# Optimization experiments

Hardware: AMD Instinct MI355X
Metric: run time of the kernel (lower is better)

Reference implementation:

```python
import jax, jax.numpy as jnp
import numpy as np

B = 8192
E = 8
H = 128
NUM_CLASSES = 3
SIM_THRESHOLD = 0.8
EFF_THRESHOLD = 0.1
TARGET_TEMP = 1.0
W_LB, W_EFF, W_CONS, W_ENT, W_TEMP = 0.1, 0.05, 0.1, 0.01, 0.01


def setup_inputs() -> dict:
    key = jax.random.key(0)
    k1, k2, k3, k4 = jax.random.split(key, 4)
    logits = jax.random.normal(k1, (B, NUM_CLASSES), dtype=jnp.float32)
    targets = jax.random.randint(k2, (B,), 0, NUM_CLASSES, dtype=jnp.int64)
    raw = jax.random.uniform(k3, (B, E), dtype=jnp.float32)
    routing_probs = raw / raw.sum(axis=-1, keepdims=True)  # rows sum to 1
    input_embeddings = jax.random.uniform(k4, (B, H), dtype=jnp.float32)
    temperature = jnp.ones((1,), dtype=jnp.float32)
    return {
        "logits": logits,
        "targets": targets,
        "routing_probs": routing_probs,
        "input_embeddings": input_embeddings,
        "temperature": temperature,
    }


def _dynamo_loss(logits, routing_probs, input_embeddings, temperature, targets):
    # --- task loss: cross entropy (sentiment) ---
    logp_cls = jax.nn.log_softmax(logits, axis=-1)
    task_loss = -jnp.take_along_axis(logp_cls, targets[:, None], axis=-1).mean()

    # --- load balance: var(mean usage) / (1/E)^2 (torch.var unbiased) ---
    expert_usage = routing_probs.mean(axis=0)  # [E]
    lb_loss = W_LB * jnp.var(expert_usage, ddof=1) * (E ** 2)

    # --- efficiency: sum of probs below threshold, averaged over batch ---
    small = jnp.where(routing_probs < EFF_THRESHOLD, routing_probs, 0.0)
    eff_loss = W_EFF * small.sum(axis=-1).mean()

    # --- consistency: masked pairwise KL over similar samples ---
    nrm = input_embeddings / jnp.linalg.norm(input_embeddings, axis=-1, keepdims=True)
    sim = nrm @ nrm.T  # [B, B]
    mask = (sim > SIM_THRESHOLD) & ~jnp.eye(B, dtype=bool)
    logp = jax.nn.log_softmax(routing_probs, axis=-1)  # [B, E]
    p = jnp.exp(logp)
    a = jnp.sum(p * logp, axis=-1)  # [B], sum_e p_j log p_j
    # KL(i,j) = sum_e p_j (log p_j - log p_i) = a[j] - logp[i] . p[j]
    kl = a[None, :] - logp @ p.T  # [B, B]
    num_pairs = mask.sum()
    kl_sum = jnp.sum(jnp.where(mask, kl, 0.0))
    cons_loss = W_CONS * jnp.where(num_pairs > 0, kl_sum / jnp.maximum(num_pairs, 1), 0.0)

    # --- entropy regularization (maximize entropy of routing_probs-as-probs) ---
    eps = 1e-8
    entropy = -jnp.sum(routing_probs * jnp.log(routing_probs + eps), axis=-1)
    ent_loss = W_ENT * (-entropy.mean())

    # --- temperature regularization ---
    temp_loss = W_TEMP * jnp.mean((temperature - TARGET_TEMP) ** 2)

    return task_loss + lb_loss + eff_loss + cons_loss + ent_loss + temp_loss


def reference(logits, targets, routing_probs, input_embeddings, temperature):
    return _dynamo_loss(logits, routing_probs, input_embeddings, temperature, targets)
```

## Files before the change

### kernel.cpp

```cpp
#include <hip/hip_runtime.h>
#include <stdint.h>

#define B_SZ 8192
#define LOG8 2.0794415416798357f
#define NTILE 2080

typedef __attribute__((ext_vector_type(8))) short short8;
typedef __attribute__((ext_vector_type(4))) float floatx4;

typedef __attribute__((address_space(1))) const uint4 guint4;
typedef __attribute__((address_space(3))) uint4 luint4;

__device__ inline void async_cp16(const uint4* g, uint4* l) {
    __builtin_amdgcn_global_load_lds((guint4*)g, (luint4*)l, 16, 0, 0);
}

__device__ inline unsigned short f2bf(float f) {
    unsigned int u = __float_as_uint(f);
    u = (u + 0x7FFFu + ((u >> 16) & 1u)) >> 16;
    return (unsigned short)u;
}
__device__ inline float bf2f(unsigned short s) {
    return __uint_as_float(((unsigned int)s) << 16);
}
__device__ inline float wredf(float x) {
#pragma unroll
    for (int o = 32; o; o >>= 1) x += __shfl_down(x, o);
    return x;
}
__device__ inline int wredi(int x) {
#pragma unroll
    for (int o = 32; o; o >>= 1) x += __shfl_down(x, o);
    return x;
}


__global__ __launch_bounds__(512) void prep_all(
    const float* __restrict__ logits,
    const int* __restrict__ targets,
    const float* __restrict__ routing,
    const float* __restrict__ emb,
    unsigned short* __restrict__ nrm,
    unsigned short* __restrict__ nlq,
    unsigned short* __restrict__ pb,
    float* __restrict__ aprime,
    float* __restrict__ prepslot) {
    __shared__ float pred[8][11];
    const int bid = blockIdx.x;
    const int lane = threadIdx.x & 63;
    const int wave = threadIdx.x >> 6;

    if (bid < 256) {
#pragma unroll
        for (int iter = 0; iter < 4; ++iter) {
            int row = (((iter << 8) + bid) << 3) + wave;
            const float2* e2 = (const float2*)(emb + (size_t)row * 128);
            float2 v = e2[lane];
            float ss = v.x * v.x + v.y * v.y;
            ss = wredf(ss);
            ss = __shfl(ss, 0);
            float inv = rsqrtf(ss);
            ushort2 o;
            o.x = f2bf(v.x * inv);
            o.y = f2bf(v.y * inv);
            ((ushort2*)(nrm + (size_t)row * 128))[lane] = o;
        }
        return;
    }

    int row = ((bid - 256) << 9) + threadIdx.x;

    const float4* r4 = (const float4*)(routing + (size_t)row * 8);
    float4 va = r4[0], vb = r4[1];
    float v[8] = {va.x, va.y, va.z, va.w, vb.x, vb.y, vb.z, vb.w};

    float mx = v[0];
#pragma unroll
    for (int e = 1; e < 8; ++e) mx = fmaxf(mx, v[e]);
    float ex[8], s = 0.f;
#pragma unroll
    for (int e = 0; e < 8; ++e) { ex[e] = expf(v[e] - mx); s += ex[e]; }
    float ls = logf(s);
    float inv_s = 1.f / s;

    union { unsigned short u[8]; uint4 q; } lu, pu;
    float ap = 0.f;
#pragma unroll
    for (int e = 0; e < 8; ++e) {
        unsigned short pe = f2bf(ex[e] * inv_s);
        unsigned short le = f2bf(v[e] - mx - ls + LOG8);
        pu.u[e] = pe;
        lu.u[e] = le ^ 0x8000;
        ap += bf2f(pe) * bf2f(le);
    }
    ((uint4*)nlq)[row] = lu.q;
    ((uint4*)pb)[row] = pu.q;
    aprime[row] = ap;

    float eff = 0.f, ent = 0.f;
#pragma unroll
    for (int e = 0; e < 8; ++e) {
        if (v[e] < 0.1f) eff += v[e];
        ent += v[e] * logf(v[e] + 1e-8f);
    }

    const float* lg = logits + (size_t)row * 3;
    float a0 = lg[0], a1 = lg[1], a2 = lg[2];
    float mm = fmaxf(a0, fmaxf(a1, a2));
    float lse = mm + logf(expf(a0 - mm) + expf(a1 - mm) + expf(a2 - mm));
    int tg = targets[row];
    float tv = (tg == 0) ? a0 : ((tg == 1) ? a1 : a2);
    float task = lse - tv;

    task = wredf(task);
    eff = wredf(eff);
    ent = wredf(ent);
    float cs[8];
#pragma unroll
    for (int e = 0; e < 8; ++e) cs[e] = wredf(v[e]);

    if (lane == 0) {
        pred[wave][0] = task;
        pred[wave][1] = eff;
        pred[wave][2] = ent;
#pragma unroll
        for (int e = 0; e < 8; ++e) pred[wave][3 + e] = cs[e];
    }
    __syncthreads();
    if (threadIdx.x < 11) {
        float s2 = 0.f;
#pragma unroll
        for (int w = 0; w < 8; ++w) s2 += pred[w][threadIdx.x];
        prepslot[(bid - 256) * 11 + threadIdx.x] = s2;
    }
}

__global__ __launch_bounds__(512, 4) void tile_sym(
    const unsigned short* __restrict__ nrm,
    const unsigned short* __restrict__ nlq,
    const unsigned short* __restrict__ pb,
    const float* __restrict__ aprime,
    float* __restrict__ klslot,
    unsigned int* __restrict__ cntslot) {
    __shared__ uint4 sh[2048];

    const int t = threadIdx.x;
    const int L = blockIdx.x;
    const int wave = t >> 6, lane = t & 63;

    int bi = (int)((129.0f - sqrtf((float)(16641 - 8 * L))) * 0.5f);
    int T = bi * 64 - ((bi * (bi - 1)) >> 1);
    while (L < T) { --bi; T = bi * 64 - ((bi * (bi - 1)) >> 1); }
    while (L >= T + (64 - bi)) { T += 64 - bi; ++bi; }
    const int bj = bi + (L - T);
    const bool diag = (bi == bj);
    const int iBase = bi << 7, jBase = bj << 7;

    const uint4* n4 = (const uint4*)nrm;

#pragma unroll
    for (int it = 0; it < 4; ++it) {
        int idx = t + (it << 9);
        int row = idx >> 4, s = idx & 15;
        int g = s ^ (row & 15);
        async_cp16(&n4[((size_t)(iBase + row) << 4) + g],
                   sh + (it << 9) + (wave << 6));
    }

    const int wr = wave >> 2, wc = wave & 3;
    const int m = lane & 15, q = lane >> 4;

    const int colB0 = jBase + (wc << 5) + m;
    short8 bfr[4][2];
#pragma unroll
    for (int ks = 0; ks < 4; ++ks)
#pragma unroll
        for (int b = 0; b < 2; ++b)
            bfr[ks][b] = *(const short8*)&nrm[(size_t)(colB0 + (b << 4)) * 128 +
                                              (ks << 5) + (q << 3)];

    __syncthreads();

    floatx4 simacc[4][2];
#pragma unroll
    for (int a = 0; a < 4; ++a)
#pragma unroll
        for (int b = 0; b < 2; ++b) simacc[a][b] = (floatx4){0.f, 0.f, 0.f, 0.f};

#pragma unroll
    for (int ks = 0; ks < 4; ++ks) {
        const int gk = (ks << 2) + q;
        short8 af[4];
#pragma unroll
        for (int a = 0; a < 4; ++a) {
            int row = (wr << 6) + (a << 4) + m;
            af[a] = *(const short8*)(sh + (row << 4) + (gk ^ m));
        }
#pragma unroll
        for (int a = 0; a < 4; ++a)
#pragma unroll
            for (int b = 0; b < 2; ++b)
                simacc[a][b] = __builtin_amdgcn_mfma_f32_16x16x32_bf16(
                    af[a], bfr[ks][b], simacc[a][b], 0, 0, 0);
    }

    const short8 zero8 = (short8){0, 0, 0, 0, 0, 0, 0, 0};
    short8 crA[4], crB[2];
#pragma unroll
    for (int a = 0; a < 4; ++a) {
        int ri = iBase + (wr << 6) + (a << 4) + m;
        short8 v = zero8;
        if (q == 0) v = *(const short8*)&nlq[(size_t)ri << 3];
        else if (q == 1) { if (!diag) v = *(const short8*)&pb[(size_t)ri << 3]; }
        else if (q == 2) {
            v[1] = (short)0x3F80;
            if (!diag) v[0] = (short)f2bf(aprime[ri]);
        }
        crA[a] = v;
    }
#pragma unroll
    for (int b = 0; b < 2; ++b) {
        int cj = jBase + (wc << 5) + (b << 4) + m;
        short8 v = zero8;
        if (q == 0) v = *(const short8*)&pb[(size_t)cj << 3];
        else if (q == 1) v = *(const short8*)&nlq[(size_t)cj << 3];
        else if (q == 2) {
            v[0] = (short)0x3F80;
            v[1] = (short)f2bf(aprime[cj]);
        }
        crB[b] = v;
    }

    float klLocal = 0.f;
    int cntLocal = 0;
#pragma unroll
    for (int a = 0; a < 4; ++a) {
        const int gRow0 = iBase + (wr << 6) + (a << 4) + (q << 2);
#pragma unroll
        for (int b = 0; b < 2; ++b) {
            const int gCol = jBase + (wc << 5) + (b << 4) + m;
            floatx4 cr = __builtin_amdgcn_mfma_f32_16x16x32_bf16(
                crA[a], crB[b], (floatx4){0.f, 0.f, 0.f, 0.f}, 0, 0, 0);
            if (diag) {
#pragma unroll
                for (int r = 0; r < 4; ++r) {
                    if ((simacc[a][b][r] > 0.8f) && (gRow0 + r != gCol)) {
                        klLocal += cr[r];
                        cntLocal += 1;
                    }
                }
            } else {
#pragma unroll
                for (int r = 0; r < 4; ++r) {
                    if (simacc[a][b][r] > 0.8f) {
                        klLocal += cr[r];
                        cntLocal += 2;
                    }
                }
            }
        }
    }

    klLocal = wredf(klLocal);
    cntLocal = wredi(cntLocal);

    __syncthreads();
    float* redk = (float*)sh;
    int* redc = (int*)(redk + 8);
    if (lane == 0) { redk[wave] = klLocal; redc[wave] = cntLocal; }
    __syncthreads();

    if (t == 0) {
        float k = 0.f;
        int c = 0;
#pragma unroll
        for (int w = 0; w < 8; ++w) { k += redk[w]; c += redc[w]; }
        klslot[L] = k;
        cntslot[L] = (unsigned int)c;
    }
}

__global__ void finalize_k(const float* __restrict__ klslot,
                           const unsigned int* __restrict__ cntslot,
                           const float* __restrict__ prepslot,
                           const float* __restrict__ temp,
                           float* __restrict__ out) {
    __shared__ float sk[4];
    __shared__ int sc[4];
    __shared__ float sp[11];
    const int t = threadIdx.x, lane = t & 63, wave = t >> 6;

    float k = 0.f;
    int c = 0;
    for (int i = t; i < NTILE; i += 256) { k += klslot[i]; c += (int)cntslot[i]; }
    k = wredf(k);
    c = wredi(c);
    if (lane == 0) { sk[wave] = k; sc[wave] = c; }
    if (t < 11) {
        float s = 0.f;
        for (int r = 0; r < 16; ++r) s += prepslot[r * 11 + t];
        sp[t] = s;
    }
    __syncthreads();
    if (t == 0) {
        float K = sk[0] + sk[1] + sk[2] + sk[3];
        int C = sc[0] + sc[1] + sc[2] + sc[3];
        const float invB = 1.f / (float)B_SZ;
        float task = sp[0] * invB;
        float eff = 0.05f * sp[1] * invB;
        float entl = 0.01f * sp[2] * invB;
        float cons = 0.1f * (C > 0 ? K / (float)C : 0.f);
        float u[8], mean = 0.f;
        for (int e = 0; e < 8; ++e) { u[e] = sp[3 + e] * invB; mean += u[e]; }
        mean *= 0.125f;
        float var = 0.f;
        for (int e = 0; e < 8; ++e) { float d = u[e] - mean; var += d * d; }
        var *= (1.f / 7.f);
        float lb = 0.1f * var * 64.f;
        float tt = temp[0] - 1.f;
        out[0] = task + lb + eff + cons + entl + 0.01f * tt * tt;
    }
}

extern "C" void kernel_launch(void* const* d_in, const int* in_sizes, int n_in,
                              void* d_out, int out_size, void* d_ws, size_t ws_size,
                              hipStream_t stream) {
    const float* logits = (const float*)d_in[0];
    const int* targets = (const int*)d_in[1];
    const float* routing = (const float*)d_in[2];
    const float* emb = (const float*)d_in[3];
    const float* temp = (const float*)d_in[4];

    char* ws = (char*)d_ws;
    unsigned short* nrm = (unsigned short*)ws;
    unsigned short* nlq = (unsigned short*)(ws + 2097152);
    unsigned short* pb = (unsigned short*)(ws + 2228224);
    float* aprime = (float*)(ws + 2359296);
    float* klslot = (float*)(ws + 2392064);
    unsigned int* cntslot = (unsigned int*)(ws + 2400384);
    float* prepslot = (float*)(ws + 2408704);

    prep_all<<<272, 512, 0, stream>>>(logits, targets, routing, emb,
                                      nrm, nlq, pb, aprime, prepslot);
    tile_sym<<<NTILE, 512, 0, stream>>>(nrm, nlq, pb, aprime, klslot, cntslot);
    finalize_k<<<1, 256, 0, stream>>>(klslot, cntslot, prepslot, temp,
                                      (float*)d_out);
}
```

Measured before the change: 107.2 us.

## Halve column tile width and stage B operand in shared memory

The symmetric tile grid changes from 128x128 tiles to 128x64 tiles, which doubles the block count. The column rows of the normalized embeddings are now loaded into LDS with async copies instead of directly into registers from global memory. Tile index decoding is rewritten for the new triangular-strip layout, with a 'strip' flag replacing the diagonal flag, and the slot offsets in the workspace are shifted to fit the larger block count. The aim is more parallelism and less register pressure, at the cost of more blocks, redundant A-tile loads, and more partial-sum slots to reduce.

```diff
diff --git a/kernel.cpp b/kernel.cpp
--- a/kernel.cpp
+++ b/kernel.cpp
@@ -3,7 +3,7 @@
 
 #define B_SZ 8192
 #define LOG8 2.0794415416798357f
-#define NTILE 2080
+#define NTILE 4160
 
 typedef __attribute__((ext_vector_type(8))) short short8;
 typedef __attribute__((ext_vector_type(4))) float floatx4;
@@ -142,19 +142,19 @@
     const float* __restrict__ aprime,
     float* __restrict__ klslot,
     unsigned int* __restrict__ cntslot) {
-    __shared__ uint4 sh[2048];
+    __shared__ uint4 sh[3072];
 
     const int t = threadIdx.x;
     const int L = blockIdx.x;
     const int wave = t >> 6, lane = t & 63;
 
-    int bi = (int)((129.0f - sqrtf((float)(16641 - 8 * L))) * 0.5f);
-    int T = bi * 64 - ((bi * (bi - 1)) >> 1);
-    while (L < T) { --bi; T = bi * 64 - ((bi * (bi - 1)) >> 1); }
-    while (L >= T + (64 - bi)) { T += 64 - bi; ++bi; }
-    const int bj = bi + (L - T);
-    const bool diag = (bi == bj);
-    const int iBase = bi << 7, jBase = bj << 7;
+    int bi = (int)((129.0f - sqrtf((float)(16641 - 4 * L))) * 0.5f);
+    int T = bi * (129 - bi);
+    while (L < T) { --bi; T = bi * (129 - bi); }
+    while (L >= T + (128 - 2 * bi)) { T += 128 - 2 * bi; ++bi; }
+    const int bj = 2 * bi + (L - T);
+    const bool strip = ((bj >> 1) == bi);
+    const int iBase = bi << 7, jBase = bj << 6;
 
     const uint4* n4 = (const uint4*)nrm;
 
@@ -166,61 +166,34 @@
         async_cp16(&n4[((size_t)(iBase + row) << 4) + g],
                    sh + (it << 9) + (wave << 6));
     }
+#pragma unroll
+    for (int it = 0; it < 2; ++it) {
+        int idx = t + (it << 9);
+        int row = idx >> 4, s = idx & 15;
+        int g = s ^ (row & 15);
+        async_cp16(&n4[((size_t)(jBase + row) << 4) + g],
+                   sh + 2048 + (it << 9) + (wave << 6));
+    }
 
     const int wr = wave >> 2, wc = wave & 3;
     const int m = lane & 15, q = lane >> 4;
-
-    const int colB0 = jBase + (wc << 5) + m;
-    short8 bfr[4][2];
-#pragma unroll
-    for (int ks = 0; ks < 4; ++ks)
-#pragma unroll
-        for (int b = 0; b < 2; ++b)
-            bfr[ks][b] = *(const short8*)&nrm[(size_t)(colB0 + (b << 4)) * 128 +
-                                              (ks << 5) + (q << 3)];
-
-    __syncthreads();
-
-    floatx4 simacc[4][2];
-#pragma unroll
-    for (int a = 0; a < 4; ++a)
-#pragma unroll
-        for (int b = 0; b < 2; ++b) simacc[a][b] = (floatx4){0.f, 0.f, 0.f, 0.f};
-
-#pragma unroll
-    for (int ks = 0; ks < 4; ++ks) {
-        const int gk = (ks << 2) + q;
-        short8 af[4];
-#pragma unroll
-        for (int a = 0; a < 4; ++a) {
-            int row = (wr << 6) + (a << 4) + m;
-            af[a] = *(const short8*)(sh + (row << 4) + (gk ^ m));
-        }
-#pragma unroll
-        for (int a = 0; a < 4; ++a)
-#pragma unroll
-            for (int b = 0; b < 2; ++b)
-                simacc[a][b] = __builtin_amdgcn_mfma_f32_16x16x32_bf16(
-                    af[a], bfr[ks][b], simacc[a][b], 0, 0, 0);
-    }
-
     const short8 zero8 = (short8){0, 0, 0, 0, 0, 0, 0, 0};
-    short8 crA[4], crB[2];
+
+    short8 crA[4], crB;
 #pragma unroll
     for (int a = 0; a < 4; ++a) {
         int ri = iBase + (wr << 6) + (a << 4) + m;
         short8 v = zero8;
         if (q == 0) v = *(const short8*)&nlq[(size_t)ri << 3];
-        else if (q == 1) { if (!diag) v = *(const short8*)&pb[(size_t)ri << 3]; }
+        else if (q == 1) { if (!strip) v = *(const short8*)&pb[(size_t)ri << 3]; }
         else if (q == 2) {
             v[1] = (short)0x3F80;
-            if (!diag) v[0] = (short)f2bf(aprime[ri]);
+            if (!strip) v[0] = (short)f2bf(aprime[ri]);
         }
         crA[a] = v;
     }
-#pragma unroll
-    for (int b = 0; b < 2; ++b) {
-        int cj = jBase + (wc << 5) + (b << 4) + m;
+    {
+        int cj = jBase + (wc << 4) + m;
         short8 v = zero8;
         if (q == 0) v = *(const short8*)&pb[(size_t)cj << 3];
         else if (q == 1) v = *(const short8*)&nlq[(size_t)cj << 3];
@@ -228,34 +201,57 @@
             v[0] = (short)0x3F80;
             v[1] = (short)f2bf(aprime[cj]);
         }
-        crB[b] = v;
+        crB = v;
+    }
+
+    __syncthreads();
+
+    floatx4 simacc[4];
+#pragma unroll
+    for (int a = 0; a < 4; ++a) simacc[a] = (floatx4){0.f, 0.f, 0.f, 0.f};
+
+#pragma unroll
+    for (int ks = 0; ks < 4; ++ks) {
+        const int gk = (ks << 2) + q;
+        short8 bfr;
+        {
+            int rb = (wc << 4) + m;
+            bfr = *(const short8*)(sh + 2048 + (rb << 4) + (gk ^ m));
+        }
+        short8 af[4];
+#pragma unroll
+        for (int a = 0; a < 4; ++a) {
+            int row = (wr << 6) + (a << 4) + m;
+            af[a] = *(const short8*)(sh + (row << 4) + (gk ^ m));
+        }
+#pragma unroll
+        for (int a = 0; a < 4; ++a)
+            simacc[a] = __builtin_amdgcn_mfma_f32_16x16x32_bf16(
+                af[a], bfr, simacc[a], 0, 0, 0);
     }
 
     float klLocal = 0.f;
     int cntLocal = 0;
+    const int gCol = jBase + (wc << 4) + m;
 #pragma unroll
     for (int a = 0; a < 4; ++a) {
         const int gRow0 = iBase + (wr << 6) + (a << 4) + (q << 2);
-#pragma unroll
-        for (int b = 0; b < 2; ++b) {
-            const int gCol = jBase + (wc << 5) + (b << 4) + m;
-            floatx4 cr = __builtin_amdgcn_mfma_f32_16x16x32_bf16(
-                crA[a], crB[b], (floatx4){0.f, 0.f, 0.f, 0.f}, 0, 0, 0);
-            if (diag) {
-#pragma unroll
-                for (int r = 0; r < 4; ++r) {
-                    if ((simacc[a][b][r] > 0.8f) && (gRow0 + r != gCol)) {
-                        klLocal += cr[r];
-                        cntLocal += 1;
-                    }
+        floatx4 cr = __builtin_amdgcn_mfma_f32_16x16x32_bf16(
+            crA[a], crB, (floatx4){0.f, 0.f, 0.f, 0.f}, 0, 0, 0);
+        if (strip) {
+#pragma unroll
+            for (int r = 0; r < 4; ++r) {
+                if ((simacc[a][r] > 0.8f) && (gRow0 + r != gCol)) {
+                    klLocal += cr[r];
+                    cntLocal += 1;
                 }
-            } else {
-#pragma unroll
-                for (int r = 0; r < 4; ++r) {
-                    if (simacc[a][b][r] > 0.8f) {
-                        klLocal += cr[r];
-                        cntLocal += 2;
-                    }
+            }
+        } else {
+#pragma unroll
+            for (int r = 0; r < 4; ++r) {
+                if (simacc[a][r] > 0.8f) {
+                    klLocal += cr[r];
+                    cntLocal += 2;
                 }
             }
         }
@@ -337,8 +333,8 @@
     unsigned short* pb = (unsigned short*)(ws + 2228224);
     float* aprime = (float*)(ws + 2359296);
     float* klslot = (float*)(ws + 2392064);
-    unsigned int* cntslot = (unsigned int*)(ws + 2400384);
-    float* prepslot = (float*)(ws + 2408704);
+    unsigned int* cntslot = (unsigned int*)(ws + 2408704);
+    float* prepslot = (float*)(ws + 2425344);
 
     prep_all<<<272, 512, 0, stream>>>(logits, targets, routing, emb,
                                       nrm, nlq, pb, aprime, prepslot);
```

Result: slower. 109.9 us (+2.5%).
